# Kernel tuning notes

Measured on AMD Instinct MI355X. Metric: run time of the kernel, lower is better.

Reference implementation:

```python
import jax, jax.numpy as jnp
import numpy as np

BATCH = 256
SEQ_LEN = 96
PRED_LEN = 96
ENC_IN = 321
D_MODEL = 512


def setup_inputs() -> dict:
    key = jax.random.key(0)
    ks = jax.random.split(key, 7)
    s = 1.0 / np.sqrt(D_MODEL)
    x_enc = jax.random.normal(ks[0], (BATCH, SEQ_LEN, ENC_IN), jnp.float32)
    Wih = jax.random.uniform(ks[1], (4 * D_MODEL, ENC_IN), jnp.float32, -s, s)
    Whh = jax.random.uniform(ks[2], (4 * D_MODEL, D_MODEL), jnp.float32, -s, s)
    bih = jax.random.uniform(ks[3], (4 * D_MODEL,), jnp.float32, -s, s)
    bhh = jax.random.uniform(ks[4], (4 * D_MODEL,), jnp.float32, -s, s)
    Wp = jax.random.uniform(ks[5], (ENC_IN, D_MODEL), jnp.float32, -s, s)
    bp = jax.random.uniform(ks[6], (ENC_IN,), jnp.float32, -s, s)
    return {"x_enc": x_enc, "Wih": Wih, "Whh": Whh, "bih": bih, "bhh": bhh, "Wp": Wp, "bp": bp}


def _lstm_step(h, c, xt, Wih, Whh, bih, bhh):
    # PyTorch LSTM gate layout: [i, f, g, o]
    g = xt @ Wih.T + h @ Whh.T + (bih + bhh)  # (B, 4*D)
    i, f, gg, o = jnp.split(g, 4, axis=-1)
    c = jax.nn.sigmoid(f) * c + jax.nn.sigmoid(i) * jnp.tanh(gg)
    h = jax.nn.sigmoid(o) * jnp.tanh(c)
    return h, c


def reference(x_enc, Wih, Whh, bih, bhh, Wp, bp):
    # Instance norm over time (use_norm=True); means detached as in torch
    means = jax.lax.stop_gradient(jnp.mean(x_enc, axis=1, keepdims=True))
    xc = x_enc - means
    stdev = jnp.sqrt(jnp.var(xc, axis=1, keepdims=True) + 1e-5)
    x = xc / stdev

    B = x.shape[0]
    h0 = jnp.zeros((B, D_MODEL), x.dtype)
    c0 = jnp.zeros((B, D_MODEL), x.dtype)

    def enc_step(carry, xt):
        h, c = carry
        h, c = _lstm_step(h, c, xt, Wih, Whh, bih, bhh)
        return (h, c), None

    (h, c), _ = jax.lax.scan(enc_step, (h0, c0), jnp.swapaxes(x, 0, 1))

    def dec_step(carry, _):
        h, c = carry
        y = h @ Wp.T + bp          # (B, ENC_IN) decoded from hidden
        h, c = _lstm_step(h, c, y, Wih, Whh, bih, bhh)
        return (h, c), y

    _, ys = jax.lax.scan(dec_step, (h, c), None, length=PRED_LEN)
    dec_out = jnp.swapaxes(ys, 0, 1)  # (B, PRED_LEN, ENC_IN)

    dec_out = dec_out * stdev[:, 0:1, :] + means[:, 0:1, :]
    return dec_out
```

## Files before the change

### kernel.cpp

```cpp
#include <hip/hip_runtime.h>
#include <hip/hip_bf16.h>
#include <math.h>

#define BB 256
#define TT 96
#define PP 96
#define CC 321
#define CP 352
#define DD 512
#define GG 2048
#define NSTEPS 191

typedef __attribute__((ext_vector_type(8))) short bf16x8;
typedef __attribute__((ext_vector_type(4))) float f32x4;
typedef __hip_bfloat16 bf16;
typedef unsigned long long u64;

__global__ void norm_kernel(const float* __restrict__ x, float* __restrict__ meanp,
                            float* __restrict__ stdp, bf16* __restrict__ xn) {
    int g = blockIdx.x * 256 + threadIdx.x;
    if (g >= BB * CC) return;
    int b = g / CC, c = g % CC;
    const float* xp = x + b * TT * CC + c;
    float s = 0.f;
    for (int t = 0; t < TT; ++t) s += xp[t * CC];
    float mu = s * (1.f / TT);
    float v = 0.f;
    for (int t = 0; t < TT; ++t) { float d0 = xp[t * CC] - mu; v += d0 * d0; }
    float sd = sqrtf(v * (1.f / TT) + 1e-5f);
    float rs = 1.f / sd;
    meanp[g] = mu;
    stdp[g] = sd;
    for (int t = 0; t < TT; ++t)
        xn[(t * BB + b) * CP + c] = __float2bfloat16((xp[t * CC] - mu) * rs);
}

__global__ void cast_pad_kernel(const float* __restrict__ src, bf16* __restrict__ dst,
                                int rows, int cols, int ldd) {
    int i = blockIdx.x * 256 + threadIdx.x;
    if (i >= rows * cols) return;
    int r = i / cols, c = i % cols;
    dst[r * ldd + c] = __float2bfloat16(src[i]);
}

__global__ void transpose_wp_kernel(const float* __restrict__ wp, bf16* __restrict__ wpt) {
    int i = blockIdx.x * 256 + threadIdx.x;
    if (i >= DD * CC) return;
    int d = i / CC, c = i % CC;
    wpt[d * CP + c] = __float2bfloat16(wp[c * DD + d]);
}

__global__ void bias_kernel(const float* __restrict__ Wih, const float* __restrict__ bih,
                            const float* __restrict__ bhh, const float* __restrict__ bp,
                            float* __restrict__ bsum, float* __restrict__ beff) {
    int j = blockIdx.x * 256 + threadIdx.x;
    if (j >= GG) return;
    float s = bih[j] + bhh[j];
    float acc = 0.f;
    const float* w = Wih + j * CC;
    for (int c = 0; c < CC; ++c) acc += w[c] * bp[c];
    bsum[j] = s;
    beff[j] = s + acc;
}

__device__ __forceinline__ void gemm_core_64x64(const bf16* A, int lda, const bf16* Bt,
                                                int ldb, int K, int m0, int n0,
                                                f32x4 acc[4]) {
    __shared__ unsigned short As[64][40];
    __shared__ unsigned short Bs[64][40];
    int tid = threadIdx.x;
    int w = tid >> 6, lane = tid & 63;
    int quad = lane >> 4, col = lane & 15;
    int lr = tid >> 2, lc = (tid & 3) * 8;
    for (int k0 = 0; k0 < K; k0 += 32) {
        __syncthreads();
        *(uint4*)&As[lr][lc] = *(const uint4*)&A[(size_t)(m0 + lr) * lda + k0 + lc];
        *(uint4*)&Bs[lr][lc] = *(const uint4*)&Bt[(size_t)(n0 + lr) * ldb + k0 + lc];
        __syncthreads();
        bf16x8 a = *(const bf16x8*)&As[w * 16 + col][quad * 8];
#pragma unroll
        for (int nt = 0; nt < 4; ++nt) {
            bf16x8 bfr = *(const bf16x8*)&Bs[nt * 16 + col][quad * 8];
            acc[nt] = __builtin_amdgcn_mfma_f32_16x16x32_bf16(a, bfr, acc[nt], 0, 0, 0);
        }
    }
}

__global__ void weff_kernel(const bf16* __restrict__ WihP, const bf16* __restrict__ WpTP,
                            const float* __restrict__ Whh, bf16* __restrict__ WeffP) {
    f32x4 acc[4] = {{0,0,0,0},{0,0,0,0},{0,0,0,0},{0,0,0,0}};
    int m0 = blockIdx.y * 64, n0 = blockIdx.x * 64;
    gemm_core_64x64(WihP, CP, WpTP, CP, CP, m0, n0, acc);
    int tid = threadIdx.x, w = tid >> 6, lane = tid & 63;
    int quad = lane >> 4, col = lane & 15;
#pragma unroll
    for (int nt = 0; nt < 4; ++nt)
#pragma unroll
        for (int r = 0; r < 4; ++r) {
            int j = m0 + w * 16 + quad * 4 + r;
            int d = n0 + nt * 16 + col;
            WeffP[j * DD + d] = __float2bfloat16(acc[nt][r] + Whh[j * DD + d]);
        }
}

__global__ void proj_kernel(const bf16* __restrict__ Hdec, const bf16* __restrict__ WpP,
                            const float* __restrict__ bp, const float* __restrict__ stdp,
                            const float* __restrict__ meanp, float* __restrict__ out) {
    f32x4 acc[4] = {{0,0,0,0},{0,0,0,0},{0,0,0,0},{0,0,0,0}};
    int m0 = blockIdx.x * 64, n0 = blockIdx.y * 64;
    gemm_core_64x64(Hdec, DD, WpP, DD, DD, m0, n0, acc);
    int tid = threadIdx.x, w = tid >> 6, lane = tid & 63;
    int quad = lane >> 4, col = lane & 15;
#pragma unroll
    for (int nt = 0; nt < 4; ++nt) {
        int c = n0 + nt * 16 + col;
        if (c >= CC) continue;
        float bpc = bp[c];
#pragma unroll
        for (int r = 0; r < 4; ++r) {
            int row = m0 + w * 16 + quad * 4 + r;
            int t = row >> 8, b = row & 255;
            float y = acc[nt][r] + bpc;
            int sc = b * CC + c;
            out[(b * PP + t) * CC + c] = y * stdp[sc] + meanp[sc];
        }
    }
}

__global__ __launch_bounds__(128, 1) void lstm_persistent(
        const bf16* __restrict__ xn,
        const bf16* __restrict__ WihP,
        const bf16* __restrict__ WhhP,
        const bf16* __restrict__ WeffP,
        const float* __restrict__ bsum, const float* __restrict__ beff,
        bf16* __restrict__ hA, bf16* __restrict__ hB,
        bf16* __restrict__ Hdec,
        unsigned int* __restrict__ bar) {
    __shared__ unsigned short Whs[4 * 16 * 16 * 32];
    __shared__ unsigned short Wxs[4 * 11 * 16 * 32];

    const int tid = threadIdx.x;
    const int w = tid >> 6, lane = tid & 63;
    const int quad = lane >> 4, col = lane & 15;
    const int dt = blockIdx.x & 31;
    const int bt = blockIdx.x >> 5;
    const int d0 = dt * 16;
    const int b0 = bt * 32;
    const int batch = b0 + w * 16 + col;

    for (int i = tid; i < 64 * 44; i += 128) {
        int row = i / 44, c8 = i % 44;
        int gt = row >> 4, cl = row & 15;
        int ki = c8 >> 2, q = c8 & 3;
        *(uint4*)&Wxs[((gt * 11 + ki) * 16 + cl) * 32 + q * 8] =
            *((const uint4*)(WihP + (size_t)(gt * DD + d0 + cl) * CP) + c8);
    }
    for (int i = tid; i < 64 * 64; i += 128) {
        int row = i >> 6, c8 = i & 63;
        int gt = row >> 4, cl = row & 15;
        int ki = c8 >> 2, q = c8 & 3;
        *(uint4*)&Whs[((gt * 16 + ki) * 16 + cl) * 32 + q * 8] =
            *((const uint4*)(WhhP + (size_t)(gt * DD + d0 + cl) * DD) + c8);
    }
    __syncthreads();

    float creg[4] = {0.f, 0.f, 0.f, 0.f};
    float bs_[16], be_[16];
#pragma unroll
    for (int g4 = 0; g4 < 16; ++g4) {
        int gt = g4 >> 2, r = g4 & 3;
        bs_[g4] = bsum[gt * DD + d0 + quad * 4 + r];
        be_[g4] = beff[gt * DD + d0 + quad * 4 + r];
    }

    unsigned int gen = 0;

    for (int s = 0; s < NSTEPS; ++s) {
        const bool enc = (s < TT);
        const bf16* h_in;
        bf16* h_out;
        if (enc) {
            h_in  = (s & 1) ? hB : hA;
            h_out = (s == TT - 1) ? Hdec : ((s & 1) ? hA : hB);
        } else {
            int td = s - TT;
            h_in  = Hdec + (size_t)td * BB * DD;
            h_out = Hdec + (size_t)(td + 1) * BB * DD;
        }

        if (s == TT) {
            for (int i = tid; i < 64 * 64; i += 128) {
                int row = i >> 6, c8 = i & 63;
                int gt = row >> 4, cl = row & 15;
                int ki = c8 >> 2, q = c8 & 3;
                *(uint4*)&Whs[((gt * 16 + ki) * 16 + cl) * 32 + q * 8] =
                    *((const uint4*)(WeffP + (size_t)(gt * DD + d0 + cl) * DD) + c8);
            }
            __syncthreads();
        }

        f32x4 acc[4] = {{0,0,0,0},{0,0,0,0},{0,0,0,0},{0,0,0,0}};

        u64 hf[32];
        {
            u64* hp = (u64*)(h_in + (size_t)batch * DD);
#pragma unroll
            for (int ki = 0; ki < 16; ++ki) {
                hf[2 * ki] = __hip_atomic_load(&hp[ki * 8 + quad * 2],
                                               __ATOMIC_RELAXED, __HIP_MEMORY_SCOPE_AGENT);
                hf[2 * ki + 1] = __hip_atomic_load(&hp[ki * 8 + quad * 2 + 1],
                                                   __ATOMIC_RELAXED, __HIP_MEMORY_SCOPE_AGENT);
            }
        }

        if (enc) {
            uint4 xf[11];
            const uint4* xp = (const uint4*)(xn + (size_t)(s * BB + batch) * CP) + quad;
#pragma unroll
            for (int ki = 0; ki < 11; ++ki) xf[ki] = xp[ki * 4];
#pragma unroll
            for (int ki = 0; ki < 11; ++ki) {
                bf16x8 xv = *(bf16x8*)&xf[ki];
#pragma unroll
                for (int gt = 0; gt < 4; ++gt) {
                    bf16x8 wf = *(const bf16x8*)&Wxs[((gt * 11 + ki) * 16 + col) * 32 + quad * 8];
                    acc[gt] = __builtin_amdgcn_mfma_f32_16x16x32_bf16(wf, xv, acc[gt], 0, 0, 0);
                }
            }
        }

#pragma unroll
        for (int ki = 0; ki < 16; ++ki) {
            union { u64 q[2]; bf16x8 v; } hu;
            hu.q[0] = hf[2 * ki];
            hu.q[1] = hf[2 * ki + 1];
#pragma unroll
            for (int gt = 0; gt < 4; ++gt) {
                bf16x8 wf = *(const bf16x8*)&Whs[((gt * 16 + ki) * 16 + col) * 32 + quad * 8];
                acc[gt] = __builtin_amdgcn_mfma_f32_16x16x32_bf16(wf, hu.v, acc[gt], 0, 0, 0);
            }
        }

        u64 pack = 0;
#pragma unroll
        for (int r = 0; r < 4; ++r) {
            float iv = acc[0][r] + (enc ? bs_[0 + r] : be_[0 + r]);
            float fv = acc[1][r] + (enc ? bs_[4 + r] : be_[4 + r]);
            float gv = acc[2][r] + (enc ? bs_[8 + r] : be_[8 + r]);
            float ov = acc[3][r] + (enc ? bs_[12 + r] : be_[12 + r]);
            float si = 1.f / (1.f + __expf(-iv));
            float sf = 1.f / (1.f + __expf(-fv));
            float so = 1.f / (1.f + __expf(-ov));
            float tg = tanhf(gv);
            float cc = sf * creg[r] + si * tg;
            creg[r] = cc;
            float hv = so * tanhf(cc);
            union { bf16 h; unsigned short u; } cv;
            cv.h = __float2bfloat16(hv);
            pack |= (u64)cv.u << (16 * r);
        }
        __hip_atomic_store((u64*)&h_out[(size_t)batch * DD + d0 + quad * 4], pack,
                           __ATOMIC_RELAXED, __HIP_MEMORY_SCOPE_AGENT);

        if (s < NSTEPS - 1) {
            ++gen;
            __builtin_amdgcn_s_waitcnt(0);
            __syncthreads();
            if (tid == 0) {
                __hip_atomic_fetch_add(&bar[bt * 32], 1u, __ATOMIC_RELAXED,
                                       __HIP_MEMORY_SCOPE_AGENT);
                unsigned int tgt = gen * 32u;
                while (__hip_atomic_load(&bar[bt * 32], __ATOMIC_RELAXED,
                                         __HIP_MEMORY_SCOPE_AGENT) < tgt)
                    __builtin_amdgcn_s_sleep(1);
            }
            __syncthreads();
        }
    }
}

extern "C" void kernel_launch(void* const* d_in, const int* in_sizes, int n_in,
                              void* d_out, int out_size, void* d_ws, size_t ws_size,
                              hipStream_t stream) {
    (void)in_sizes; (void)n_in; (void)out_size;
    const float* x_enc = (const float*)d_in[0];
    const float* Wih   = (const float*)d_in[1];
    const float* Whh   = (const float*)d_in[2];
    const float* bih   = (const float*)d_in[3];
    const float* bhh   = (const float*)d_in[4];
    const float* Wp    = (const float*)d_in[5];
    const float* bp    = (const float*)d_in[6];
    float* out = (float*)d_out;

    char* ws = (char*)d_ws;
    size_t off = 0;
    float* meanp = (float*)(ws + off); off += (size_t)BB * CC * 4;
    float* stdp  = (float*)(ws + off); off += (size_t)BB * CC * 4;
    bf16* xnormP = (bf16*)(ws + off);  off += (size_t)TT * BB * CP * 2;
    bf16* WihP   = (bf16*)(ws + off);  off += (size_t)GG * CP * 2;
    bf16* WhhP   = (bf16*)(ws + off);  off += (size_t)GG * DD * 2;
    bf16* WeffP  = (bf16*)(ws + off);  off += (size_t)GG * DD * 2;
    bf16* WpTP   = (bf16*)(ws + off);  off += (size_t)DD * CP * 2;
    bf16* WpP    = (bf16*)(ws + off);  off += (size_t)384 * DD * 2;
    float* bsum  = (float*)(ws + off); off += (size_t)GG * 4;
    float* beff  = (float*)(ws + off); off += (size_t)GG * 4;
    bf16* hA     = (bf16*)(ws + off);  off += (size_t)BB * DD * 2;
    bf16* hB     = (bf16*)(ws + off);  off += (size_t)BB * DD * 2;
    bf16* Hdec   = (bf16*)(ws + off);  off += (size_t)PP * BB * DD * 2;
    unsigned int* bar = (unsigned int*)(ws + off); off += 1024;
    if (ws_size < off) return;

    hipMemsetAsync(xnormP, 0, (size_t)TT * BB * CP * 2, stream);
    hipMemsetAsync(WihP,   0, (size_t)GG * CP * 2, stream);
    hipMemsetAsync(WpTP,   0, (size_t)DD * CP * 2, stream);
    hipMemsetAsync(WpP,    0, (size_t)384 * DD * 2, stream);
    hipMemsetAsync(hA,     0, (size_t)BB * DD * 2, stream);
    hipMemsetAsync(bar,    0, 1024, stream);

    norm_kernel<<<(BB * CC + 255) / 256, 256, 0, stream>>>(x_enc, meanp, stdp, xnormP);
    cast_pad_kernel<<<(GG * CC + 255) / 256, 256, 0, stream>>>(Wih, WihP, GG, CC, CP);
    cast_pad_kernel<<<(GG * DD + 255) / 256, 256, 0, stream>>>(Whh, WhhP, GG, DD, DD);
    cast_pad_kernel<<<(CC * DD + 255) / 256, 256, 0, stream>>>(Wp, WpP, CC, DD, DD);
    transpose_wp_kernel<<<(DD * CC + 255) / 256, 256, 0, stream>>>(Wp, WpTP);
    bias_kernel<<<GG / 256, 256, 0, stream>>>(Wih, bih, bhh, bp, bsum, beff);
    weff_kernel<<<dim3(DD / 64, GG / 64), 256, 0, stream>>>(WihP, WpTP, Whh, WeffP);

    const bf16* xn_c = xnormP;  const bf16* wih_c = WihP;
    const bf16* whh_c = WhhP;   const bf16* weff_c = WeffP;
    const float* bs_c = bsum;   const float* be_c = beff;
    bf16* hA_c = hA; bf16* hB_c = hB; bf16* hd_c = Hdec; unsigned int* bar_c = bar;
    void* args[] = {&xn_c, &wih_c, &whh_c, &weff_c, &bs_c, &be_c,
                    &hA_c, &hB_c, &hd_c, &bar_c};
    hipLaunchCooperativeKernel((void*)lstm_persistent, dim3(256), dim3(128),
                               args, 0, stream);

    proj_kernel<<<dim3(PP * BB / 64, 384 / 64), 256, 0, stream>>>(
        Hdec, WpP, bp, stdp, meanp, out);
}
```

Measured before the change: 1.383 ms.

## Replace per-step group barrier with poison-value dataflow sync on hidden state

Removes the per-step atomic counter barrier among the 32 blocks sharing a batch tile. Each step now writes its hidden state to a fresh slot in a full time-history buffer that was pre-filled with 0xFF. Consumers spin-reload any 64-bit word that still holds the poison value. This cuts barrier round-trips and lets blocks proceed as soon as their inputs arrive. In exchange it adds memsets of about 25MB of history buffers and relies on a real bf16x4 output never equalling all-ones (NaN) and on relaxed-ordering visibility.

```diff
diff --git a/kernel.cpp b/kernel.cpp
--- a/kernel.cpp
+++ b/kernel.cpp
@@ -10,6 +10,7 @@
 #define DD 512
 #define GG 2048
 #define NSTEPS 191
+#define POISON 0xFFFFFFFFFFFFFFFFull
 
 typedef __attribute__((ext_vector_type(8))) short bf16x8;
 typedef __attribute__((ext_vector_type(4))) float f32x4;
@@ -133,9 +134,8 @@
         const bf16* __restrict__ WhhP,
         const bf16* __restrict__ WeffP,
         const float* __restrict__ bsum, const float* __restrict__ beff,
-        bf16* __restrict__ hA, bf16* __restrict__ hB,
-        bf16* __restrict__ Hdec,
-        unsigned int* __restrict__ bar) {
+        bf16* __restrict__ hEnc,
+        bf16* __restrict__ Hdec) {
     __shared__ unsigned short Whs[4 * 16 * 16 * 32];
     __shared__ unsigned short Wxs[4 * 11 * 16 * 32];
 
@@ -173,15 +173,13 @@
         be_[g4] = beff[gt * DD + d0 + quad * 4 + r];
     }
 
-    unsigned int gen = 0;
-
     for (int s = 0; s < NSTEPS; ++s) {
         const bool enc = (s < TT);
         const bf16* h_in;
         bf16* h_out;
         if (enc) {
-            h_in  = (s & 1) ? hB : hA;
-            h_out = (s == TT - 1) ? Hdec : ((s & 1) ? hA : hB);
+            h_in  = hEnc + (size_t)s * BB * DD;
+            h_out = (s == TT - 1) ? Hdec : hEnc + (size_t)(s + 1) * BB * DD;
         } else {
             int td = s - TT;
             h_in  = Hdec + (size_t)td * BB * DD;
@@ -189,6 +187,7 @@
         }
 
         if (s == TT) {
+            __syncthreads();
             for (int i = tid; i < 64 * 64; i += 128) {
                 int row = i >> 6, c8 = i & 63;
                 int gt = row >> 4, cl = row & 15;
@@ -210,6 +209,19 @@
                                                __ATOMIC_RELAXED, __HIP_MEMORY_SCOPE_AGENT);
                 hf[2 * ki + 1] = __hip_atomic_load(&hp[ki * 8 + quad * 2 + 1],
                                                    __ATOMIC_RELAXED, __HIP_MEMORY_SCOPE_AGENT);
+            }
+            while (true) {
+                bool bad = false;
+#pragma unroll
+                for (int k = 0; k < 32; ++k) bad |= (hf[k] == POISON);
+                if (!__any(bad)) break;
+                __builtin_amdgcn_s_sleep(1);
+#pragma unroll
+                for (int k = 0; k < 32; ++k)
+                    if (hf[k] == POISON)
+                        hf[k] = __hip_atomic_load(&hp[(k >> 1) * 8 + quad * 2 + (k & 1)],
+                                                  __ATOMIC_RELAXED,
+                                                  __HIP_MEMORY_SCOPE_AGENT);
             }
         }
 
@@ -261,21 +273,6 @@
         }
         __hip_atomic_store((u64*)&h_out[(size_t)batch * DD + d0 + quad * 4], pack,
                            __ATOMIC_RELAXED, __HIP_MEMORY_SCOPE_AGENT);
-
-        if (s < NSTEPS - 1) {
-            ++gen;
-            __builtin_amdgcn_s_waitcnt(0);
-            __syncthreads();
-            if (tid == 0) {
-                __hip_atomic_fetch_add(&bar[bt * 32], 1u, __ATOMIC_RELAXED,
-                                       __HIP_MEMORY_SCOPE_AGENT);
-                unsigned int tgt = gen * 32u;
-                while (__hip_atomic_load(&bar[bt * 32], __ATOMIC_RELAXED,
-                                         __HIP_MEMORY_SCOPE_AGENT) < tgt)
-                    __builtin_amdgcn_s_sleep(1);
-            }
-            __syncthreads();
-        }
     }
 }
 
@@ -304,18 +301,18 @@
     bf16* WpP    = (bf16*)(ws + off);  off += (size_t)384 * DD * 2;
     float* bsum  = (float*)(ws + off); off += (size_t)GG * 4;
     float* beff  = (float*)(ws + off); off += (size_t)GG * 4;
-    bf16* hA     = (bf16*)(ws + off);  off += (size_t)BB * DD * 2;
-    bf16* hB     = (bf16*)(ws + off);  off += (size_t)BB * DD * 2;
+    bf16* hEnc   = (bf16*)(ws + off);  off += (size_t)TT * BB * DD * 2;
     bf16* Hdec   = (bf16*)(ws + off);  off += (size_t)PP * BB * DD * 2;
-    unsigned int* bar = (unsigned int*)(ws + off); off += 1024;
     if (ws_size < off) return;
 
     hipMemsetAsync(xnormP, 0, (size_t)TT * BB * CP * 2, stream);
     hipMemsetAsync(WihP,   0, (size_t)GG * CP * 2, stream);
     hipMemsetAsync(WpTP,   0, (size_t)DD * CP * 2, stream);
     hipMemsetAsync(WpP,    0, (size_t)384 * DD * 2, stream);
-    hipMemsetAsync(hA,     0, (size_t)BB * DD * 2, stream);
-    hipMemsetAsync(bar,    0, 1024, stream);
+    hipMemsetAsync(hEnc,   0, (size_t)BB * DD * 2, stream);
+    hipMemsetAsync(hEnc + (size_t)BB * DD, 0xFF,
+                   (size_t)(TT - 1) * BB * DD * 2, stream);
+    hipMemsetAsync(Hdec, 0xFF, (size_t)PP * BB * DD * 2, stream);
 
     norm_kernel<<<(BB * CC + 255) / 256, 256, 0, stream>>>(x_enc, meanp, stdp, xnormP);
     cast_pad_kernel<<<(GG * CC + 255) / 256, 256, 0, stream>>>(Wih, WihP, GG, CC, CP);
@@ -328,9 +325,8 @@
     const bf16* xn_c = xnormP;  const bf16* wih_c = WihP;
     const bf16* whh_c = WhhP;   const bf16* weff_c = WeffP;
     const float* bs_c = bsum;   const float* be_c = beff;
-    bf16* hA_c = hA; bf16* hB_c = hB; bf16* hd_c = Hdec; unsigned int* bar_c = bar;
-    void* args[] = {&xn_c, &wih_c, &whh_c, &weff_c, &bs_c, &be_c,
-                    &hA_c, &hB_c, &hd_c, &bar_c};
+    bf16* he_c = hEnc; bf16* hd_c = Hdec;
+    void* args[] = {&xn_c, &wih_c, &whh_c, &weff_c, &bs_c, &be_c, &he_c, &hd_c};
     hipLaunchCooperativeKernel((void*)lstm_persistent, dim3(256), dim3(128),
                                args, 0, stream);
 
```

Measured after the change: 1.796 ms. 1.3x slower.
